# Kernel optimization log

Hardware: AMD Instinct MI355X
Metric: run time of the kernel (lower is better)

## Reference

```python
import jax, jax.numpy as jnp
import numpy as np

N = 50000   # nodes
E = 800000  # edges
IN, HID, OUT = 128, 128, 64


def setup_inputs() -> dict:
    key = jax.random.key(0)
    ks = jax.random.split(key, 16)
    x = jax.random.normal(ks[0], (N, IN), dtype=jnp.float32)
    src = jax.random.randint(ks[1], (E,), 0, N, dtype=jnp.int32)
    dst = jax.random.randint(ks[2], (E,), 0, N, dtype=jnp.int32)
    s = 1.0 / np.sqrt(IN)
    W_self1 = jax.random.normal(ks[3], (IN, HID), dtype=jnp.float32) * s
    W_neigh1 = jax.random.normal(ks[4], (IN, HID), dtype=jnp.float32) * s
    b1 = jnp.zeros((HID,), dtype=jnp.float32)
    W_self2 = jax.random.normal(ks[5], (HID, HID), dtype=jnp.float32) * s
    W_neigh2 = jax.random.normal(ks[6], (HID, HID), dtype=jnp.float32) * s
    b2 = jnp.zeros((HID,), dtype=jnp.float32)
    W_self3 = jax.random.normal(ks[7], (HID, OUT), dtype=jnp.float32) * s
    W_neigh3 = jax.random.normal(ks[8], (HID, OUT), dtype=jnp.float32) * s
    b3 = jnp.zeros((OUT,), dtype=jnp.float32)
    # dropout(p=0.5) masks, pre-scaled by 1/(1-p)
    keep = 0.5
    mask1 = (jax.random.uniform(ks[9], (N, HID)) < keep).astype(jnp.float32) / keep
    mask2 = (jax.random.uniform(ks[10], (N, HID)) < keep).astype(jnp.float32) / keep
    return dict(x=x, src=src, dst=dst,
                W_self1=W_self1, W_neigh1=W_neigh1, b1=b1,
                W_self2=W_self2, W_neigh2=W_neigh2, b2=b2,
                W_self3=W_self3, W_neigh3=W_neigh3, b3=b3,
                mask1=mask1, mask2=mask2)


def _mean_agg(h, src, dst):
    # gather source features, segment-sum into destinations, divide by in-degree
    summed = jax.ops.segment_sum(h[src], dst, num_segments=N)  # [N, d]
    deg = jax.ops.segment_sum(jnp.ones((E,), dtype=h.dtype), dst, num_segments=N)
    return summed / jnp.maximum(deg, 1.0)[:, None]


def _sage_layer(h, src, dst, W_self, W_neigh, b):
    h_neigh = _mean_agg(h, src, dst)
    return h @ W_self + h_neigh @ W_neigh + b


def reference(x, src, dst, W_self1, W_neigh1, b1, W_self2, W_neigh2, b2,
              W_self3, W_neigh3, b3, mask1, mask2):
    h = _sage_layer(x, src, dst, W_self1, W_neigh1, b1)
    h = jax.nn.relu(h) * mask1
    h = _sage_layer(h, src, dst, W_self2, W_neigh2, b2)
    h = jax.nn.relu(h) * mask2
    h = _sage_layer(h, src, dst, W_self3, W_neigh3, b3)
    return h
```

## Files before the change

kernel.cpp:

```cpp
#include <hip/hip_runtime.h>
#include <hip/hip_bf16.h>

#define DIN  128
#define DHID 128
#define DOUT 64

#define EB   2048
#define CAPB 5120

typedef short short8 __attribute__((ext_vector_type(8)));
typedef float f32x4  __attribute__((ext_vector_type(4)));

__device__ __forceinline__ ushort f2bf(float f) {
    union { float f; uint u; } c; c.f = f;
    uint u = c.u;
    return (ushort)((u + 0x7fff + ((u >> 16) & 1)) >> 16);
}
__device__ __forceinline__ float bf2f(uint h16) {
    union { uint u; float f; } c; c.u = h16 << 16;
    return c.f;
}
__device__ __forceinline__ float sb8(uint u, int k) {
    return (float)((int)(u << (24 - 8 * k)) >> 24);
}

__device__ __forceinline__ void wprep_dev(const float* __restrict__ W,
                                          ushort* __restrict__ Wt, int OUT, int idx) {
    int nn = idx >> 7;
    int k  = idx & 127;
    Wt[idx] = f2bf(W[(size_t)k * OUT + nn]);
}

__global__ __launch_bounds__(256)
void megaprep(const int* __restrict__ src, const int* __restrict__ dst, int E, int fillB,
              int* __restrict__ bkt_cur, uint* __restrict__ pairs,
              const float* __restrict__ x, ushort* __restrict__ xb, int n4, int cvtB,
              const float* __restrict__ Ws1, const float* __restrict__ Wn1,
              const float* __restrict__ Ws2, const float* __restrict__ Wn2,
              const float* __restrict__ Ws3, const float* __restrict__ Wn3,
              ushort* __restrict__ Wst1, ushort* __restrict__ Wnt1,
              ushort* __restrict__ Wst2, ushort* __restrict__ Wnt2,
              ushort* __restrict__ Wst3, ushort* __restrict__ Wnt3) {
    __shared__ int c[256];
    __shared__ int startl[256];
    __shared__ int ofs[256];
    int b = blockIdx.x;
    const int t = threadIdx.x;
    if (b < fillB) {
        c[t] = 0;
        __syncthreads();
        const int base = b * EB;
        const int end = min(base + EB, E);
        for (int i = base + t; i < end; i += 256)
            atomicAdd(&c[dst[i] >> 8], 1);
        __syncthreads();
        int v = c[t];
        startl[t] = v ? (t * CAPB + atomicAdd(&bkt_cur[t], v)) : 0;
        ofs[t] = 0;
        __syncthreads();
        for (int i = base + t; i < end; i += 256) {
            int d = dst[i];
            int bb = d >> 8;
            int p = startl[bb] + atomicAdd(&ofs[bb], 1);
            pairs[p] = ((uint)src[i] << 8) | (uint)(d & 255);
        }
        return;
    }
    b -= fillB;
    if (b < cvtB) {
        int i = b * 256 + t;
        if (i < n4) {
            float4 v = ((const float4*)x)[i];
            ushort4 o;
            o.x = f2bf(v.x); o.y = f2bf(v.y); o.z = f2bf(v.z); o.w = f2bf(v.w);
            ((ushort4*)xb)[i] = o;
        }
        return;
    }
    b -= cvtB;
    if (b < 64)  { wprep_dev(Ws1, Wst1, 128, b * 256 + t); return; }
    b -= 64;
    if (b < 64)  { wprep_dev(Wn1, Wnt1, 128, b * 256 + t); return; }
    b -= 64;
    if (b < 64)  { wprep_dev(Ws2, Wst2, 128, b * 256 + t); return; }
    b -= 64;
    if (b < 64)  { wprep_dev(Wn2, Wnt2, 128, b * 256 + t); return; }
    b -= 64;
    if (b < 32)  { wprep_dev(Ws3, Wst3, 64, b * 256 + t); return; }
    b -= 32;
    wprep_dev(Wn3, Wnt3, 64, b * 256 + t);
}

__global__ __launch_bounds__(1024)
void bucket_csr(const uint* __restrict__ pairs, const int* __restrict__ bkt_cur,
                int* __restrict__ row_ptr, int* __restrict__ deg,
                int* __restrict__ esrc, int N, int nbkt) {
    constexpr int CAP = 6144;
    __shared__ uint pl[CAP];
    __shared__ int cnt[256];
    __shared__ int rs[256];
    __shared__ int sc[256];
    const int bkt = blockIdx.x;
    const int t = threadIdx.x;
    const int ebase = bkt * CAPB;
    const int ecnt  = min(bkt_cur[bkt], CAPB);
    if (t < 256) cnt[t] = 0;
    __syncthreads();
    const bool fits = (ecnt <= CAP);
    if (fits) {
        for (int i = t; i < ecnt; i += 1024) {
            uint p = pairs[ebase + i];
            pl[i] = p;
            atomicAdd(&cnt[p & 255u], 1);
        }
    } else {
        for (int i = t; i < ecnt; i += 1024)
            atomicAdd(&cnt[pairs[ebase + i] & 255u], 1);
    }
    __syncthreads();
    int own = 0;
    if (t < 256) { own = cnt[t]; sc[t] = own; }
    __syncthreads();
    for (int o = 1; o < 256; o <<= 1) {
        int u = (t < 256 && t >= o) ? sc[t - o] : 0;
        __syncthreads();
        if (t < 256) sc[t] += u;
        __syncthreads();
    }
    if (t < 256) {
        rs[t] = sc[t] - own;
        const int node = bkt * 256 + t;
        if (node < N) {
            row_ptr[node] = ebase + rs[t];
            deg[node] = own;
        }
    }
    __syncthreads();
    if (fits) {
        for (int i = t; i < ecnt; i += 1024) {
            uint p = pl[i];
            int pos = atomicAdd(&rs[p & 255u], 1);
            esrc[ebase + pos] = (int)(p >> 8);
        }
    } else {
        for (int i = t; i < ecnt; i += 1024) {
            uint p = pairs[ebase + i];
            int pos = atomicAdd(&rs[p & 255u], 1);
            esrc[ebase + pos] = (int)(p >> 8);
        }
    }
}

template<int OUTW>
__global__ __launch_bounds__(256)
void sage_gemm(const ushort* __restrict__ Hb,
               const ushort* __restrict__ Wst,
               const ushort* __restrict__ Wnt,
               ushort* __restrict__ S,
               signed char* __restrict__ Gq,
               float* __restrict__ Gsc,
               int n) {
    constexpr int NT = OUTW / 16;
    __shared__ ushort Wl[2][OUTW * 128];

    const int tid  = threadIdx.x;
    const int lane = tid & 63;
    const int wave = tid >> 6;
    const int rg   = wave >> 1;
    const int isG  = wave & 1;
    const int m16  = lane & 15;
    const int kb   = lane >> 4;
    const int rbase = blockIdx.x * 64 + rg * 32;

    {
        const uint4* s4 = (const uint4*)Wst;
        const uint4* n4 = (const uint4*)Wnt;
        uint4* ls = (uint4*)&Wl[0][0];
        uint4* ln = (uint4*)&Wl[1][0];
#pragma unroll
        for (int j = tid; j < OUTW * 128 / 8; j += 256) {
            ls[j] = s4[j];
            ln[j] = n4[j];
        }
    }

    short8 a[2][4];
#pragma unroll
    for (int mt = 0; mt < 2; ++mt) {
        int arow = rbase + mt * 16 + m16;
        if (arow >= n) arow = n - 1;
        const ushort* __restrict__ Ap = &Hb[(size_t)arow * 128 + kb * 8];
#pragma unroll
        for (int c = 0; c < 4; ++c)
            a[mt][c] = *(const short8*)(Ap + c * 32);
    }

    __syncthreads();

    f32x4 acc[2][NT];
#pragma unroll
    for (int mt = 0; mt < 2; ++mt)
#pragma unroll
        for (int t = 0; t < NT; ++t) acc[mt][t] = (f32x4)(0.f);

    const ushort* __restrict__ Wp = &Wl[isG][0];
#pragma unroll
    for (int t = 0; t < NT; ++t) {
#pragma unroll
        for (int c = 0; c < 4; ++c) {
            short8 b = *(const short8*)&Wp[(t * 16 + m16) * 128 + c * 32 + kb * 8];
            acc[0][t] = __builtin_amdgcn_mfma_f32_16x16x32_bf16(a[0][c], b, acc[0][t], 0, 0, 0);
            acc[1][t] = __builtin_amdgcn_mfma_f32_16x16x32_bf16(a[1][c], b, acc[1][t], 0, 0, 0);
        }
    }

#pragma unroll
    for (int mt = 0; mt < 2; ++mt) {
        const int rb = rbase + mt * 16;
        if (!isG) {
#pragma unroll
            for (int r = 0; r < 4; ++r) {
                int row = rb + kb * 4 + r;
                if (row >= n) continue;
#pragma unroll
                for (int t = 0; t < NT; ++t)
                    S[(size_t)row * OUTW + t * 16 + m16] = f2bf(acc[mt][t][r]);
            }
        } else {
#pragma unroll
            for (int r = 0; r < 4; ++r) {
                float mx = 0.f;
#pragma unroll
                for (int t = 0; t < NT; ++t) mx = fmaxf(mx, fabsf(acc[mt][t][r]));
                mx = fmaxf(mx, __shfl_xor(mx, 1));
                mx = fmaxf(mx, __shfl_xor(mx, 2));
                mx = fmaxf(mx, __shfl_xor(mx, 4));
                mx = fmaxf(mx, __shfl_xor(mx, 8));
                int row = rb + kb * 4 + r;
                if (row >= n) continue;
                float inv = (mx > 0.f) ? 127.f / mx : 0.f;
                if (m16 == 0) Gsc[row] = mx * (1.f / 127.f);
#pragma unroll
                for (int t = 0; t < NT; ++t) {
                    int q = (int)rintf(acc[mt][t][r] * inv);
                    q = max(-127, min(127, q));
                    Gq[(size_t)row * OUTW + t * 16 + m16] = (signed char)q;
                }
            }
        }
    }
}

__device__ __forceinline__ void acc8(float* af, uint2 v, float sc) {
    af[0] += sc * sb8(v.x, 0); af[1] += sc * sb8(v.x, 1);
    af[2] += sc * sb8(v.x, 2); af[3] += sc * sb8(v.x, 3);
    af[4] += sc * sb8(v.y, 0); af[5] += sc * sb8(v.y, 1);
    af[6] += sc * sb8(v.y, 2); af[7] += sc * sb8(v.y, 3);
}
__device__ __forceinline__ void acc16(float* af, uint4 v, float sc) {
    af[0]  += sc * sb8(v.x, 0); af[1]  += sc * sb8(v.x, 1);
    af[2]  += sc * sb8(v.x, 2); af[3]  += sc * sb8(v.x, 3);
    af[4]  += sc * sb8(v.y, 0); af[5]  += sc * sb8(v.y, 1);
    af[6]  += sc * sb8(v.y, 2); af[7]  += sc * sb8(v.y, 3);
    af[8]  += sc * sb8(v.z, 0); af[9]  += sc * sb8(v.z, 1);
    af[10] += sc * sb8(v.z, 2); af[11] += sc * sb8(v.z, 3);
    af[12] += sc * sb8(v.w, 0); af[13] += sc * sb8(v.w, 1);
    af[14] += sc * sb8(v.w, 2); af[15] += sc * sb8(v.w, 3);
}

#define WCAP 320

#define LOADT16(V, C, j_)                                           \
    _Pragma("unroll")                                               \
    for (int k = 0; k < 4; ++k) {                                   \
        int p_ = i0 + (j_) * 4 + k;                                 \
        bool ok_ = p_ < e_;                                         \
        uint2 pr_ = iw[ok_ ? p_ : i0];                              \
        V[k] = *(const uint4*)&gp[(size_t)pr_.x * 128];             \
        C[k] = ok_ ? __uint_as_float(pr_.y) : 0.f;                  \
    }
#define LOADT8(V, C, j_)                                            \
    _Pragma("unroll")                                               \
    for (int k = 0; k < 4; ++k) {                                   \
        int p_ = i0 + (j_) * 4 + k;                                 \
        bool ok_ = p_ < e_;                                         \
        uint2 pr_ = iw[ok_ ? p_ : i0];                              \
        V[k] = *(const uint2*)&gp[(size_t)pr_.x * 64];              \
        C[k] = ok_ ? __uint_as_float(pr_.y) : 0.f;                  \
    }
#define CONST16(V, C)                                               \
    _Pragma("unroll") for (int k = 0; k < 4; ++k) acc16(af, V[k], C[k]);
#define CONST8(V, C)                                                \
    _Pragma("unroll") for (int k = 0; k < 4; ++k) acc8(af, V[k], C[k]);

template<bool FINAL>
__global__ __launch_bounds__(128)
void sage_gather(const signed char* __restrict__ Gq, const float* __restrict__ Gsc,
                 const ushort* __restrict__ S, const float* __restrict__ bias,
                 const float* __restrict__ mask,
                 const int* __restrict__ row_ptr, const int* __restrict__ deg,
                 const int* __restrict__ esrc,
                 void* __restrict__ outv, int n) {
    __shared__ uint2 is_s[2][WCAP];

    const int tid  = threadIdx.x;
    const int wave = tid >> 6;
    const int lane = tid & 63;
    const int g    = lane >> 3;
    const int l8   = lane & 7;
    const int wbase = blockIdx.x * 16 + wave * 8;
    if (wbase >= n) return;

    const int node = wbase + g;
    int d = 0, rp = 0;
    if (node < n) { d = deg[node]; rp = row_ptr[node]; }

    const int last   = min(wbase + 7, n - 1);
    const int span_s = row_ptr[wbase];
    const int span_e = row_ptr[last] + deg[last];
    const int len    = span_e - span_s;
    uint2* __restrict__ iw = is_s[wave];
    const bool staged = (len <= WCAP);
    if (staged) {
        int sA[5];
#pragma unroll
        for (int r = 0; r < 5; ++r) {
            int i = lane + r * 64;
            sA[r] = (i < len) ? esrc[span_s + i] : 0;
        }
#pragma unroll
        for (int r = 0; r < 5; ++r) {
            int i = lane + r * 64;
            if (i < len)
                iw[i] = make_uint2((uint)sA[r], __float_as_uint(Gsc[sA[r]]));
        }
    }

    if (node >= n) return;
    const float inv = 1.f / fmaxf((float)d, 1.f);

    if (!FINAL) {
        float af[16];
#pragma unroll
        for (int q = 0; q < 16; ++q) af[q] = 0.f;
        const signed char* __restrict__ gp = Gq + l8 * 16;
        const int col0 = l8 * 16;

        uint4 sa = *(const uint4*)&S[(size_t)node * 128 + col0];
        uint4 sb = *(const uint4*)&S[(size_t)node * 128 + col0 + 8];
        float bv[16], mv[16];
#pragma unroll
        for (int q = 0; q < 4; ++q) {
            *(float4*)&bv[q * 4] = *(const float4*)&bias[col0 + q * 4];
            *(float4*)&mv[q * 4] = *(const float4*)&mask[(size_t)node * 128 + col0 + q * 4];
        }

        if (staged) {
            const int i0 = rp - span_s;
            const int e_ = i0 + d;
            const int nb = (d + 3) >> 2;
            uint4 vA[4], vB[4], vC[4]; float cA[4], cB[4], cC[4];
            if (nb > 0) {
                LOADT16(vA, cA, 0);
                if (nb > 1) { LOADT16(vB, cB, 1); }
                if (nb > 2) { LOADT16(vC, cC, 2); }
                int b = 0;
                while (true) {
                    CONST16(vA, cA);
                    if (b + 3 < nb) { LOADT16(vA, cA, b + 3); }
                    ++b; if (b >= nb) break;
                    CONST16(vB, cB);
                    if (b + 3 < nb) { LOADT16(vB, cB, b + 3); }
                    ++b; if (b >= nb) break;
                    CONST16(vC, cC);
                    if (b + 3 < nb) { LOADT16(vC, cC, b + 3); }
                    ++b; if (b >= nb) break;
                }
            }
        } else {
            int i = rp, e = i + d;
            for (; i < e; ++i) {
                int ns = esrc[i];
                acc16(af, *(const uint4*)&gp[(size_t)ns * 128], Gsc[ns]);
            }
        }
        uint sv[8] = {sa.x, sa.y, sa.z, sa.w, sb.x, sb.y, sb.z, sb.w};
        uint pk[8];
#pragma unroll
        for (int q = 0; q < 8; ++q) {
            float z0 = bf2f(sv[q] & 0xffffu) + af[2 * q]     * inv + bv[2 * q];
            float z1 = bf2f(sv[q] >> 16)     + af[2 * q + 1] * inv + bv[2 * q + 1];
            z0 = fmaxf(z0, 0.f) * mv[2 * q];
            z1 = fmaxf(z1, 0.f) * mv[2 * q + 1];
            pk[q] = (uint)f2bf(z0) | ((uint)f2bf(z1) << 16);
        }
        ushort* op = (ushort*)outv + (size_t)node * 128 + col0;
        uint4 o0, o1;
        o0.x = pk[0]; o0.y = pk[1]; o0.z = pk[2]; o0.w = pk[3];
        o1.x = pk[4]; o1.y = pk[5]; o1.z = pk[6]; o1.w = pk[7];
        *(uint4*)op = o0;
        *(uint4*)(op + 8) = o1;
    } else {
        float af[8];
#pragma unroll
        for (int q = 0; q < 8; ++q) af[q] = 0.f;
        const signed char* __restrict__ gp = Gq + l8 * 8;
        const int col0 = l8 * 8;

        uint4 sv4 = *(const uint4*)&S[(size_t)node * 64 + col0];
        float bv[8];
        *(float4*)&bv[0] = *(const float4*)&bias[col0];
        *(float4*)&bv[4] = *(const float4*)&bias[col0 + 4];

        if (staged) {
            const int i0 = rp - span_s;
            const int e_ = i0 + d;
            const int nb = (d + 3) >> 2;
            uint2 vA[4], vB[4], vC[4]; float cA[4], cB[4], cC[4];
            if (nb > 0) {
                LOADT8(vA, cA, 0);
                if (nb > 1) { LOADT8(vB, cB, 1); }
                if (nb > 2) { LOADT8(vC, cC, 2); }
                int b = 0;
                while (true) {
                    CONST8(vA, cA);
                    if (b + 3 < nb) { LOADT8(vA, cA, b + 3); }
                    ++b; if (b >= nb) break;
                    CONST8(vB, cB);
                    if (b + 3 < nb) { LOADT8(vB, cB, b + 3); }
                    ++b; if (b >= nb) break;
                    CONST8(vC, cC);
                    if (b + 3 < nb) { LOADT8(vC, cC, b + 3); }
                    ++b; if (b >= nb) break;
                }
            }
        } else {
            int i = rp, e = i + d;
            for (; i < e; ++i) {
                int ns = esrc[i];
                acc8(af, *(const uint2*)&gp[(size_t)ns * 64], Gsc[ns]);
            }
        }
        uint sv[4] = {sv4.x, sv4.y, sv4.z, sv4.w};
        float z[8];
#pragma unroll
        for (int q = 0; q < 4; ++q) {
            z[2 * q]     = bf2f(sv[q] & 0xffffu) + af[2 * q]     * inv + bv[2 * q];
            z[2 * q + 1] = bf2f(sv[q] >> 16)     + af[2 * q + 1] * inv + bv[2 * q + 1];
        }
        float* op = (float*)outv + (size_t)node * 64 + col0;
        float4 o0, o1;
        o0.x = z[0]; o0.y = z[1]; o0.z = z[2]; o0.w = z[3];
        o1.x = z[4]; o1.y = z[5]; o1.z = z[6]; o1.w = z[7];
        *(float4*)&op[0] = o0;
        *(float4*)&op[4] = o1;
    }
}

extern "C" void kernel_launch(void* const* d_in, const int* in_sizes, int n_in,
                              void* d_out, int out_size, void* d_ws, size_t ws_size,
                              hipStream_t stream) {
    const float* x   = (const float*)d_in[0];
    const int*   src = (const int*)d_in[1];
    const int*   dst = (const int*)d_in[2];
    const float* Ws1 = (const float*)d_in[3];
    const float* Wn1 = (const float*)d_in[4];
    const float* b1  = (const float*)d_in[5];
    const float* Ws2 = (const float*)d_in[6];
    const float* Wn2 = (const float*)d_in[7];
    const float* b2  = (const float*)d_in[8];
    const float* Ws3 = (const float*)d_in[9];
    const float* Wn3 = (const float*)d_in[10];
    const float* b3  = (const float*)d_in[11];
    const float* mask1 = (const float*)d_in[12];
    const float* mask2 = (const float*)d_in[13];
    float* out = (float*)d_out;

    const int N = in_sizes[0] / DIN;
    const int E = in_sizes[1];
    const int nbkt = (N + 255) >> 8;

    char* ws = (char*)d_ws;
    int* bkt_cur  = (int*)ws;
    int* row_ptr  = bkt_cur + 256;
    int* deg      = row_ptr + N;
    int* esrc     = deg + N;
    size_t off = ((size_t)(256 + 2 * N + nbkt * CAPB) * sizeof(int) + 255) & ~(size_t)255;
    uint* pairs  = (uint*)(ws + off);    off += (size_t)nbkt * CAPB * 4;
    ushort* xb   = (ushort*)(ws + off);  off += (size_t)N * 128 * 2;
    ushort* h1b  = (ushort*)(ws + off);  off += (size_t)N * 128 * 2;
    ushort* h2b  = (ushort*)(ws + off);  off += (size_t)N * 128 * 2;
    ushort* S    = (ushort*)(ws + off);  off += (size_t)N * 128 * 2;
    signed char* Gq = (signed char*)(ws + off); off += (size_t)N * 128;
    float* Gsc   = (float*)(ws + off);   off += (size_t)N * 4;
    ushort* Wst1 = (ushort*)(ws + off);  off += 128 * 128 * 2;
    ushort* Wnt1 = (ushort*)(ws + off);  off += 128 * 128 * 2;
    ushort* Wst2 = (ushort*)(ws + off);  off += 128 * 128 * 2;
    ushort* Wnt2 = (ushort*)(ws + off);  off += 128 * 128 * 2;
    ushort* Wst3 = (ushort*)(ws + off);  off += 64 * 128 * 2;
    ushort* Wnt3 = (ushort*)(ws + off);  off += 64 * 128 * 2;

    const int n4 = N * 128 / 4;
    const int cvtB = (n4 + 255) / 256;
    const int fillB = (E + EB - 1) / EB;

    hipMemsetAsync(bkt_cur, 0, 256 * sizeof(int), stream);
    megaprep<<<fillB + cvtB + 4 * 64 + 2 * 32, 256, 0, stream>>>(
        src, dst, E, fillB, bkt_cur, pairs,
        x, xb, n4, cvtB,
        Ws1, Wn1, Ws2, Wn2, Ws3, Wn3,
        Wst1, Wnt1, Wst2, Wnt2, Wst3, Wnt3);

    bucket_csr<<<nbkt, 1024, 0, stream>>>(pairs, bkt_cur, row_ptr, deg, esrc, N, nbkt);

    const int gemmB = (N + 63) / 64;
    const int gathB = (N + 15) / 16;

    sage_gemm<128><<<gemmB, 256, 0, stream>>>(xb, Wst1, Wnt1, S, Gq, Gsc, N);
    sage_gather<false><<<gathB, 128, 0, stream>>>(Gq, Gsc, S, b1, mask1, row_ptr, deg, esrc, h1b, N);
    sage_gemm<128><<<gemmB, 256, 0, stream>>>(h1b, Wst2, Wnt2, S, Gq, Gsc, N);
    sage_gather<false><<<gathB, 128, 0, stream>>>(Gq, Gsc, S, b2, mask2, row_ptr, deg, esrc, h2b, N);
    sage_gemm<64><<<gemmB, 256, 0, stream>>>(h2b, Wst3, Wnt3, S, Gq, Gsc, N);
    sage_gather<true><<<gathB, 128, 0, stream>>>(Gq, Gsc, S, b3, nullptr, row_ptr, deg, esrc, out, N);
}
```

Baseline: 272.7 us.

## Merge CSR bucket build with layer-1 GEMM in one launch; register-cache edges in fill

The CSR bucket-sorting kernel and the first-layer GEMM are independent, so they now run as a single launch with block ranges split by blockIdx. This removes one kernel launch and lets the GEMM blocks overlap with the atomic-heavy CSR blocks. The GEMM part is re-tiled to 1024-thread blocks covering 256 rows, with four 256-thread sub-blocks sharing one LDS copy of the weights. Separately, the edge-fill pass loads each full chunk's src/dst into registers once instead of reading dst twice from global memory. The cost is a 64KB LDS footprint and 1024-thread blocks, which may limit occupancy for the CSR part.

```diff
diff --git a/kernel.cpp b/kernel.cpp
--- a/kernel.cpp
+++ b/kernel.cpp
@@ -51,18 +51,41 @@
         __syncthreads();
         const int base = b * EB;
         const int end = min(base + EB, E);
-        for (int i = base + t; i < end; i += 256)
-            atomicAdd(&c[dst[i] >> 8], 1);
-        __syncthreads();
-        int v = c[t];
-        startl[t] = v ? (t * CAPB + atomicAdd(&bkt_cur[t], v)) : 0;
-        ofs[t] = 0;
-        __syncthreads();
-        for (int i = base + t; i < end; i += 256) {
-            int d = dst[i];
-            int bb = d >> 8;
-            int p = startl[bb] + atomicAdd(&ofs[bb], 1);
-            pairs[p] = ((uint)src[i] << 8) | (uint)(d & 255);
+        if (end - base == EB) {
+            int dl[8], sl[8];
+#pragma unroll
+            for (int r = 0; r < 8; ++r) {
+                dl[r] = dst[base + t + r * 256];
+                sl[r] = src[base + t + r * 256];
+            }
+#pragma unroll
+            for (int r = 0; r < 8; ++r) atomicAdd(&c[dl[r] >> 8], 1);
+            __syncthreads();
+            int v = c[t];
+            startl[t] = v ? (t * CAPB + atomicAdd(&bkt_cur[t], v)) : 0;
+            ofs[t] = 0;
+            __syncthreads();
+#pragma unroll
+            for (int r = 0; r < 8; ++r) {
+                int d = dl[r];
+                int bb = d >> 8;
+                int p = startl[bb] + atomicAdd(&ofs[bb], 1);
+                pairs[p] = ((uint)sl[r] << 8) | (uint)(d & 255);
+            }
+        } else {
+            for (int i = base + t; i < end; i += 256)
+                atomicAdd(&c[dst[i] >> 8], 1);
+            __syncthreads();
+            int v = c[t];
+            startl[t] = v ? (t * CAPB + atomicAdd(&bkt_cur[t], v)) : 0;
+            ofs[t] = 0;
+            __syncthreads();
+            for (int i = base + t; i < end; i += 256) {
+                int d = dst[i];
+                int bb = d >> 8;
+                int p = startl[bb] + atomicAdd(&ofs[bb], 1);
+                pairs[p] = ((uint)src[i] << 8) | (uint)(d & 255);
+            }
         }
         return;
     }
@@ -92,61 +115,164 @@
 }
 
 __global__ __launch_bounds__(1024)
-void bucket_csr(const uint* __restrict__ pairs, const int* __restrict__ bkt_cur,
-                int* __restrict__ row_ptr, int* __restrict__ deg,
-                int* __restrict__ esrc, int N, int nbkt) {
-    constexpr int CAP = 6144;
-    __shared__ uint pl[CAP];
-    __shared__ int cnt[256];
-    __shared__ int rs[256];
-    __shared__ int sc[256];
-    const int bkt = blockIdx.x;
-    const int t = threadIdx.x;
-    const int ebase = bkt * CAPB;
-    const int ecnt  = min(bkt_cur[bkt], CAPB);
-    if (t < 256) cnt[t] = 0;
+void csr_gemm1(const uint* __restrict__ pairs, const int* __restrict__ bkt_cur,
+               int* __restrict__ row_ptr, int* __restrict__ deg,
+               int* __restrict__ esrc, int N, int nbkt,
+               const ushort* __restrict__ Hb,
+               const ushort* __restrict__ Wst, const ushort* __restrict__ Wnt,
+               ushort* __restrict__ S, signed char* __restrict__ Gq,
+               float* __restrict__ Gsc) {
+    __shared__ __align__(16) char smem[65536];
+    const int tid = threadIdx.x;
+    int b = blockIdx.x;
+
+    if (b < nbkt) {
+        constexpr int CAP = 6144;
+        uint* pl  = (uint*)smem;
+        int*  cnt = (int*)(smem + 24576);
+        int*  rs  = (int*)(smem + 25600);
+        int*  sc  = (int*)(smem + 26624);
+        const int bkt = b;
+        const int ebase = bkt * CAPB;
+        const int ecnt  = min(bkt_cur[bkt], CAPB);
+        if (tid < 256) cnt[tid] = 0;
+        __syncthreads();
+        const bool fits = (ecnt <= CAP);
+        if (fits) {
+            for (int i = tid; i < ecnt; i += 1024) {
+                uint p = pairs[ebase + i];
+                pl[i] = p;
+                atomicAdd(&cnt[p & 255u], 1);
+            }
+        } else {
+            for (int i = tid; i < ecnt; i += 1024)
+                atomicAdd(&cnt[pairs[ebase + i] & 255u], 1);
+        }
+        __syncthreads();
+        int own = 0;
+        if (tid < 256) { own = cnt[tid]; sc[tid] = own; }
+        __syncthreads();
+        for (int o = 1; o < 256; o <<= 1) {
+            int u = (tid < 256 && tid >= o) ? sc[tid - o] : 0;
+            __syncthreads();
+            if (tid < 256) sc[tid] += u;
+            __syncthreads();
+        }
+        if (tid < 256) {
+            rs[tid] = sc[tid] - own;
+            const int node = bkt * 256 + tid;
+            if (node < N) {
+                row_ptr[node] = ebase + rs[tid];
+                deg[node] = own;
+            }
+        }
+        __syncthreads();
+        if (fits) {
+            for (int i = tid; i < ecnt; i += 1024) {
+                uint p = pl[i];
+                int pos = atomicAdd(&rs[p & 255u], 1);
+                esrc[ebase + pos] = (int)(p >> 8);
+            }
+        } else {
+            for (int i = tid; i < ecnt; i += 1024) {
+                uint p = pairs[ebase + i];
+                int pos = atomicAdd(&rs[p & 255u], 1);
+                esrc[ebase + pos] = (int)(p >> 8);
+            }
+        }
+        return;
+    }
+
+    b -= nbkt;
+    constexpr int OUTW = 128;
+    constexpr int NT = OUTW / 16;
+    ushort* Wl = (ushort*)smem;
+
+    {
+        const uint4* s4 = (const uint4*)Wst;
+        const uint4* n4 = (const uint4*)Wnt;
+        uint4* ls = (uint4*)Wl;
+        uint4* ln = (uint4*)(Wl + OUTW * 128);
+#pragma unroll
+        for (int j = tid; j < OUTW * 128 / 8; j += 1024) {
+            ls[j] = s4[j];
+            ln[j] = n4[j];
+        }
+    }
+
+    const int vb   = tid >> 8;
+    const int t2   = tid & 255;
+    const int lane = t2 & 63;
+    const int rg   = t2 >> 7;
+    const int isG  = (t2 >> 6) & 1;
+    const int m16  = lane & 15;
+    const int kb   = lane >> 4;
+    const int rbase = b * 256 + vb * 64 + rg * 32;
+    const int n = N;
+
+    short8 a[2][4];
+#pragma unroll
+    for (int mt = 0; mt < 2; ++mt) {
+        int arow = rbase + mt * 16 + m16;
+        if (arow >= n) arow = n - 1;
+        const ushort* __restrict__ Ap = &Hb[(size_t)arow * 128 + kb * 8];
+#pragma unroll
+        for (int c = 0; c < 4; ++c)
+            a[mt][c] = *(const short8*)(Ap + c * 32);
+    }
+
     __syncthreads();
-    const bool fits = (ecnt <= CAP);
-    if (fits) {
-        for (int i = t; i < ecnt; i += 1024) {
-            uint p = pairs[ebase + i];
-            pl[i] = p;
-            atomicAdd(&cnt[p & 255u], 1);
-        }
-    } else {
-        for (int i = t; i < ecnt; i += 1024)
-            atomicAdd(&cnt[pairs[ebase + i] & 255u], 1);
-    }
-    __syncthreads();
-    int own = 0;
-    if (t < 256) { own = cnt[t]; sc[t] = own; }
-    __syncthreads();
-    for (int o = 1; o < 256; o <<= 1) {
-        int u = (t < 256 && t >= o) ? sc[t - o] : 0;
-        __syncthreads();
-        if (t < 256) sc[t] += u;
-        __syncthreads();
-    }
-    if (t < 256) {
-        rs[t] = sc[t] - own;
-        const int node = bkt * 256 + t;
-        if (node < N) {
-            row_ptr[node] = ebase + rs[t];
-            deg[node] = own;
-        }
-    }
-    __syncthreads();
-    if (fits) {
-        for (int i = t; i < ecnt; i += 1024) {
-            uint p = pl[i];
-            int pos = atomicAdd(&rs[p & 255u], 1);
-            esrc[ebase + pos] = (int)(p >> 8);
-        }
-    } else {
-        for (int i = t; i < ecnt; i += 1024) {
-            uint p = pairs[ebase + i];
-            int pos = atomicAdd(&rs[p & 255u], 1);
-            esrc[ebase + pos] = (int)(p >> 8);
+
+    f32x4 acc[2][NT];
+#pragma unroll
+    for (int mt = 0; mt < 2; ++mt)
+#pragma unroll
+        for (int t = 0; t < NT; ++t) acc[mt][t] = (f32x4)(0.f);
+
+    const ushort* __restrict__ Wp = &Wl[isG * OUTW * 128];
+#pragma unroll
+    for (int t = 0; t < NT; ++t) {
+#pragma unroll
+        for (int c = 0; c < 4; ++c) {
+            short8 bb = *(const short8*)&Wp[(t * 16 + m16) * 128 + c * 32 + kb * 8];
+            acc[0][t] = __builtin_amdgcn_mfma_f32_16x16x32_bf16(a[0][c], bb, acc[0][t], 0, 0, 0);
+            acc[1][t] = __builtin_amdgcn_mfma_f32_16x16x32_bf16(a[1][c], bb, acc[1][t], 0, 0, 0);
+        }
+    }
+
+#pragma unroll
+    for (int mt = 0; mt < 2; ++mt) {
+        const int rb = rbase + mt * 16;
+        if (!isG) {
+#pragma unroll
+            for (int r = 0; r < 4; ++r) {
+                int row = rb + kb * 4 + r;
+                if (row >= n) continue;
+#pragma unroll
+                for (int t = 0; t < NT; ++t)
+                    S[(size_t)row * OUTW + t * 16 + m16] = f2bf(acc[mt][t][r]);
+            }
+        } else {
+#pragma unroll
+            for (int r = 0; r < 4; ++r) {
+                float mx = 0.f;
+#pragma unroll
+                for (int t = 0; t < NT; ++t) mx = fmaxf(mx, fabsf(acc[mt][t][r]));
+                mx = fmaxf(mx, __shfl_xor(mx, 1));
+                mx = fmaxf(mx, __shfl_xor(mx, 2));
+                mx = fmaxf(mx, __shfl_xor(mx, 4));
+                mx = fmaxf(mx, __shfl_xor(mx, 8));
+                int row = rb + kb * 4 + r;
+                if (row >= n) continue;
+                float inv = (mx > 0.f) ? 127.f / mx : 0.f;
+                if (m16 == 0) Gsc[row] = mx * (1.f / 127.f);
+#pragma unroll
+                for (int t = 0; t < NT; ++t) {
+                    int q = (int)rintf(acc[mt][t][r] * inv);
+                    q = max(-127, min(127, q));
+                    Gq[(size_t)row * OUTW + t * 16 + m16] = (signed char)q;
+                }
+            }
         }
     }
 }
@@ -511,12 +637,14 @@
         Ws1, Wn1, Ws2, Wn2, Ws3, Wn3,
         Wst1, Wnt1, Wst2, Wnt2, Wst3, Wnt3);
 
-    bucket_csr<<<nbkt, 1024, 0, stream>>>(pairs, bkt_cur, row_ptr, deg, esrc, N, nbkt);
+    const int g256 = (N + 255) / 256;
+    csr_gemm1<<<nbkt + g256, 1024, 0, stream>>>(
+        pairs, bkt_cur, row_ptr, deg, esrc, N, nbkt,
+        xb, Wst1, Wnt1, S, Gq, Gsc);
 
     const int gemmB = (N + 63) / 64;
     const int gathB = (N + 15) / 16;
 
-    sage_gemm<128><<<gemmB, 256, 0, stream>>>(xb, Wst1, Wnt1, S, Gq, Gsc, N);
     sage_gather<false><<<gathB, 128, 0, stream>>>(Gq, Gsc, S, b1, mask1, row_ptr, deg, esrc, h1b, N);
     sage_gemm<128><<<gemmB, 256, 0, stream>>>(h1b, Wst2, Wnt2, S, Gq, Gsc, N);
     sage_gather<false><<<gathB, 128, 0, stream>>>(Gq, Gsc, S, b2, mask2, row_ptr, deg, esrc, h2b, N);
```

Result: faster. 266.7 us (-2.2%).
